# Optimization experiments

Measured on AMD Instinct MI355X. Metric: run time of the kernel, lower is better.

## Reference

```python
import jax, jax.numpy as jnp
import numpy as np

N_HEAD = 16

def rel_shift(x):
    # x: (qlen, klen, B, n). Pad one zero column at front of klen axis,
    # reinterpret as (klen+1, qlen, B, n), drop first row, reshape back.
    qlen, klen, b, n = x.shape
    x_pad = jnp.pad(x, ((0, 0), (1, 0), (0, 0), (0, 0)))
    x_pad = x_pad.reshape(klen + 1, qlen, b, n)
    return x_pad[1:].reshape(qlen, klen, b, n)

def setup_inputs() -> dict:
    key = jax.random.key(0)
    ks = jax.random.split(key, 9)
    qlen = klen = 1024
    B = 4
    d_model = 1024
    d_head = d_model // N_HEAD
    q = jax.random.normal(ks[0], (qlen, B, d_model), jnp.float32)
    K = jax.random.normal(ks[1], (klen, B, d_model), jnp.float32)
    V = jax.random.normal(ks[2], (klen, B, d_model), jnp.float32)
    mask = jax.random.bernoulli(ks[3], 0.1, (1, klen, B, 1))
    r = jax.random.normal(ks[4], (klen, d_model), jnp.float32)
    u = jax.random.normal(ks[5], (N_HEAD, d_head), jnp.float32) * 0.02
    v = jax.random.normal(ks[6], (N_HEAD, d_head), jnp.float32) * 0.02
    Wr = jax.random.normal(ks[7], (d_model, d_model), jnp.float32) / np.sqrt(d_model)
    br = jax.random.normal(ks[8], (d_model,), jnp.float32) * 0.02
    return {"q": q, "K": K, "V": V, "mask": mask, "r": r, "u": u, "v": v, "Wr": Wr, "br": br}

def reference(q, K, V, mask, r, u, v, Wr, br):
    qlen, bsz, d_model = q.shape
    klen = K.shape[0]
    d_head = d_model // N_HEAD
    qh = q.reshape(qlen, bsz, N_HEAD, d_head)
    Kh = K.reshape(klen, bsz, N_HEAD, d_head)
    Vh = V.reshape(klen, bsz, N_HEAD, d_head)
    rh = (r @ Wr.T + br).reshape(klen, N_HEAD, d_head)  # r_net projection
    AC = jnp.einsum('ibnd,jbnd->ijbn', qh + u, Kh)
    BD = rel_shift(jnp.einsum('ibnd,jnd->ijbn', qh + v, rh))
    score = (AC + BD) / jnp.sqrt(jnp.asarray(d_head, q.dtype))
    # mask (1,klen,B,1) broadcasts over qlen and heads (torch repeats over heads)
    score = jnp.where(mask, jnp.asarray(-1e9, score.dtype), score)
    weight = jax.nn.softmax(score, axis=1)
    out = jnp.einsum('ijbn,jbnd->ibnd', weight, Vh).reshape(qlen, bsz, d_model)
    return out, weight.mean(axis=-1)
```

## Files before the change

kernel.cpp:

```cpp
#include <hip/hip_runtime.h>
#include <hip/hip_fp16.h>
#include <stdint.h>


#define L 1024
#define BATCH 4
#define NH 16
#define DH 64
#define DM 1024
#define TI 16
#define NJT 16
#define BDP_ST 1032
#define SCALE 0.125f

typedef __attribute__((ext_vector_type(8))) short short8;
typedef __attribute__((ext_vector_type(4))) float f32x4;

static __device__ __forceinline__ unsigned short f2bf(float f) {
    union { float f; unsigned int u; } x; x.f = f;
    return (unsigned short)((x.u + 0x7fffu + ((x.u >> 16) & 1u)) >> 16);
}
static __device__ __forceinline__ float bf2f(unsigned short h) {
    union { unsigned int u; float f; } x; x.u = ((unsigned int)h) << 16;
    return x.f;
}
static __device__ __forceinline__ unsigned short f2h(float f) {
    __half h = __float2half(f);
    union { __half h; unsigned short s; } x; x.h = h; return x.s;
}
static __device__ __forceinline__ float h2f(unsigned short s) {
    union { __half h; unsigned short s; } x; x.s = s; return __half2float(x.h);
}
static __device__ __forceinline__ unsigned short* usp(void* base, int byteoff) {
    return (unsigned short*)((char*)base + byteoff);
}
static __device__ __forceinline__ short8 ld8(const void* base, int byteoff) {
    return *(const short8*)((const char*)base + byteoff);
}
#define SW128(row, colByte) ((((row) * 128) + (colByte)) ^ (((row) & 7) << 4))

__global__ __launch_bounds__(256) void rh_gemm_kernel(
    const float* __restrict__ r, const float* __restrict__ Wr,
    const float* __restrict__ br, float* __restrict__ rhf,
    unsigned short* __restrict__ rhb, int bfmode)
{
    __shared__ float As[16][65];
    __shared__ float Bs[16][65];
    const int j0 = blockIdx.x * 64;
    const int m0 = blockIdx.y * 64;
    const int tid = threadIdx.x;
    const int ty = tid >> 4, tx = tid & 15;
    float acc[4][4] = {};

    for (int k0 = 0; k0 < DM; k0 += 16) {
        const int row = tid >> 2, c4 = (tid & 3) << 2;
        float4 av = *(const float4*)(r  + (size_t)(j0 + row) * DM + k0 + c4);
        float4 bv = *(const float4*)(Wr + (size_t)(m0 + row) * DM + k0 + c4);
        __syncthreads();
        As[c4 + 0][row] = av.x; As[c4 + 1][row] = av.y;
        As[c4 + 2][row] = av.z; As[c4 + 3][row] = av.w;
        Bs[c4 + 0][row] = bv.x; Bs[c4 + 1][row] = bv.y;
        Bs[c4 + 2][row] = bv.z; Bs[c4 + 3][row] = bv.w;
        __syncthreads();
#pragma unroll
        for (int k = 0; k < 16; ++k) {
            float a[4], bb[4];
#pragma unroll
            for (int t = 0; t < 4; ++t) { a[t] = As[k][ty * 4 + t]; bb[t] = Bs[k][tx * 4 + t]; }
#pragma unroll
            for (int ii = 0; ii < 4; ++ii)
#pragma unroll
                for (int jj = 0; jj < 4; ++jj)
                    acc[ii][jj] = fmaf(a[ii], bb[jj], acc[ii][jj]);
        }
    }
#pragma unroll
    for (int ii = 0; ii < 4; ++ii) {
        const int row = j0 + ty * 4 + ii;
#pragma unroll
        for (int jj = 0; jj < 4; ++jj) {
            const int col = m0 + tx * 4 + jj;
            const float val = acc[ii][jj] + br[col];
            if (bfmode)
                rhb[(((size_t)(col >> 6)) * L + row) * DH + (col & 63)] = f2bf(val);
            else
                rhf[(size_t)row * DM + col] = val;
        }
    }
}

__global__ __launch_bounds__(256) void prepass_kernel(
    const float* __restrict__ Kg, const float* __restrict__ Vg,
    unsigned short* __restrict__ Kbf, unsigned short* __restrict__ Vtb)
{
    __shared__ unsigned short tile[64][80];
    const int j0 = blockIdx.x * 64;
    const int b = blockIdx.y, n = blockIdx.z;
    const int bn = b * NH + n;
    const int tid = threadIdx.x;

    for (int idx = tid; idx < 64 * 16; idx += 256) {
        const int jr = idx >> 4, s4 = (idx & 15) * 4;
        const size_t src = ((size_t)(j0 + jr) * BATCH + b) * DM + n * DH + s4;
        float4 kv = *(const float4*)(Kg + src);
        ushort4 o;
        o.x = f2bf(kv.x); o.y = f2bf(kv.y); o.z = f2bf(kv.z); o.w = f2bf(kv.w);
        *(ushort4*)(Kbf + ((size_t)bn * L + j0 + jr) * DH + s4) = o;
        float4 vv4 = *(const float4*)(Vg + src);
        tile[s4 + 0][jr] = f2bf(vv4.x); tile[s4 + 1][jr] = f2bf(vv4.y);
        tile[s4 + 2][jr] = f2bf(vv4.z); tile[s4 + 3][jr] = f2bf(vv4.w);
    }
    __syncthreads();
    for (int idx = tid; idx < 64 * 8; idx += 256) {
        const int d = idx >> 3, p8 = (idx & 7) * 8;
        short8 o = *(const short8*)&tile[d][p8];
        *(short8*)(Vtb + ((size_t)bn * DH + d) * L + j0 + p8) = o;
    }
}

__global__ __launch_bounds__(256) void wm_reduce_kernel(
    const unsigned short* __restrict__ W_ws, float* __restrict__ wm_out)
{
    const int gi = blockIdx.x;
    const int b  = blockIdx.y;
    const int j0 = threadIdx.x * 4;
    float acc0 = 0.f, acc1 = 0.f, acc2 = 0.f, acc3 = 0.f;
#pragma unroll
    for (int n = 0; n < NH; ++n) {
        ushort4 wv = *(const ushort4*)(W_ws + (((size_t)(b * NH + n) * L + gi) * L) + j0);
        acc0 += bf2f(wv.x); acc1 += bf2f(wv.y);
        acc2 += bf2f(wv.z); acc3 += bf2f(wv.w);
    }
    const size_t o = ((size_t)gi * L + j0) * BATCH + b;
    wm_out[o]             = acc0 * (1.f / 16.f);
    wm_out[o + BATCH]     = acc1 * (1.f / 16.f);
    wm_out[o + 2 * BATCH] = acc2 * (1.f / 16.f);
    wm_out[o + 3 * BATCH] = acc3 * (1.f / 16.f);
}

template<int MODE, int PLAIN>
__global__ __launch_bounds__(256, 2) void attn_kernel(
    const float* __restrict__ q,
    const void* __restrict__ Kp, const void* __restrict__ Vp,
    const unsigned char* __restrict__ maskp,
    const float* __restrict__ uu, const float* __restrict__ vvp,
    const void* __restrict__ rhp,
    float* __restrict__ out, float* __restrict__ wm_out,
    unsigned short* __restrict__ W_ws)
{
    __shared__ unsigned short QU[16 * 64];
    __shared__ unsigned short QV[17 * 64];
    __shared__ unsigned short KR[(MODE == 1) ? 64 * 64 : 8];
    __shared__ unsigned short VT[(MODE == 1) ? 64 * 64 : 8];
    __shared__ unsigned short BDp[17 * BDP_ST];
    __shared__ unsigned short Wt[16 * 64];
    __shared__ unsigned char mblk[L];
    __shared__ float denomP[4][16];
    __shared__ float rdenom[16];
    __shared__ int mflags;

    const int i0 = blockIdx.x * TI;
    const int b  = blockIdx.y;
    const int n  = blockIdx.z;
    const int bn = b * NH + n;
    const int tid = threadIdx.x;
    const int w = tid >> 6, lane = tid & 63, lr = lane & 15, lg = lane >> 4;

    const unsigned short* Kbf = (const unsigned short*)Kp;
    const unsigned short* Vtb = (const unsigned short*)Vp;
    const unsigned short* rhb = (const unsigned short*)rhp;
    const float* Kg  = (const float*)Kp;
    const float* Vg  = (const float*)Vp;
    const float* rhf = (const float*)rhp;

    if (tid == 0) mflags = 0;
    __syncthreads();
    {
        int local = 0;
        for (int ww = tid; ww < 1024; ww += 256) {
            const unsigned int word = ((const unsigned int*)maskp)[ww];
            if (word == 0x3f800000u) local |= 1;
            else if (word & 0xffffff00u) local |= 2;
        }
        if (local) atomicOr(&mflags, local);
    }
    __syncthreads();
    {
        const int mtype = (mflags & 1) ? 2 : ((mflags & 2) ? 1 : 0);
        for (int j = tid; j < L; j += 256) {
            bool mv;
            if (mtype == 2)      mv = ((const float*)maskp)[j * BATCH + b] != 0.f;
            else if (mtype == 1) mv = maskp[j * BATCH + b] != 0;
            else                 mv = ((const int*)maskp)[j * BATCH + b] != 0;
            mblk[j] = mv ? 1 : 0;
        }
    }
    for (int idx = tid; idx < 17 * 64; idx += 256) {
        const int row = idx >> 6, d = idx & 63;
        const int gi = i0 + row;
        const float qval = (gi < L) ? q[((size_t)gi * BATCH + b) * DM + n * DH + d] : 0.f;
        *usp(QV, SW128(row, d * 2)) = f2bf(qval + vvp[n * DH + d]);
        if (row < 16) *usp(QU, SW128(row, d * 2)) = f2bf(qval + uu[n * DH + d]);
    }
    __syncthreads();

    for (int ct = 0; ct < 16; ++ct) {
        const int c0 = ct * 64;
        if constexpr (MODE == 1) {
            __syncthreads();
            for (int idx = tid; idx < 64 * 16; idx += 256) {
                const int cr = idx >> 4, d4 = (idx & 15) * 4;
                float4 rv = *(const float4*)(rhf + (size_t)(c0 + cr) * DM + n * DH + d4);
                unsigned short* p = usp(KR, SW128(cr, d4 * 2));
                p[0] = f2bf(rv.x); p[1] = f2bf(rv.y); p[2] = f2bf(rv.z); p[3] = f2bf(rv.w);
            }
            __syncthreads();
        }
        const int ccol = w * 16 + lr;
        f32x4 acc = {0.f, 0.f, 0.f, 0.f};
#pragma unroll
        for (int kh = 0; kh < 2; ++kh) {
            short8 a = ld8(QV, SW128(lr, (kh * 32 + lg * 8) * 2));
            short8 bb;
            if constexpr (MODE == 0)
                bb = *(const short8*)(rhb + ((size_t)n * L + c0 + ccol) * DH + kh * 32 + lg * 8);
            else
                bb = ld8(KR, SW128(ccol, (kh * 32 + lg * 8) * 2));
            acc = __builtin_amdgcn_mfma_f32_16x16x32_bf16(a, bb, acc, 0, 0, 0);
        }
#pragma unroll
        for (int r2 = 0; r2 < 4; ++r2)
            BDp[(lg * 4 + r2) * BDP_ST + c0 + ccol] = f2h(acc[r2]);
        {
            const int col = tid >> 2, kq = (tid & 3) * 16;
            float s16 = 0.f;
#pragma unroll
            for (int kk = 0; kk < 16; kk += 8) {
                short8 qa = ld8(QV, SW128(16, (kq + kk) * 2));
                short8 ra;
                if constexpr (MODE == 0)
                    ra = *(const short8*)(rhb + ((size_t)n * L + c0 + col) * DH + kq + kk);
                else
                    ra = ld8(KR, SW128(col, (kq + kk) * 2));
#pragma unroll
                for (int e = 0; e < 8; ++e)
                    s16 = fmaf(bf2f((unsigned short)qa[e]), bf2f((unsigned short)ra[e]), s16);
            }
            s16 += __shfl_xor(s16, 1);
            s16 += __shfl_xor(s16, 2);
            if ((tid & 3) == 0) BDp[16 * BDP_ST + c0 + col] = f2h(s16);
        }
    }
    __syncthreads();

    f32x4 pv = {0.f, 0.f, 0.f, 0.f};
    float dl[4] = {0.f, 0.f, 0.f, 0.f};
    float tmp[4][NJT];
    const int jloc = w * 16 + lr;
#pragma unroll
    for (int jt = 0; jt < NJT; ++jt) {
        const int j0 = jt * 64;
        const int gj = j0 + jloc;
        if constexpr (MODE == 1) {
            for (int idx = tid; idx < 64 * 16; idx += 256) {
                const int jr = idx >> 4, d4 = (idx & 15) * 4;
                const size_t src = ((size_t)(j0 + jr) * BATCH + b) * DM + n * DH + d4;
                float4 kv = *(const float4*)(Kg + src);
                unsigned short* p = usp(KR, SW128(jr, d4 * 2));
                p[0] = f2bf(kv.x); p[1] = f2bf(kv.y); p[2] = f2bf(kv.z); p[3] = f2bf(kv.w);
                float4 vv4 = *(const float4*)(Vg + src);
                *usp(VT, SW128(d4 + 0, jr * 2)) = f2bf(vv4.x);
                *usp(VT, SW128(d4 + 1, jr * 2)) = f2bf(vv4.y);
                *usp(VT, SW128(d4 + 2, jr * 2)) = f2bf(vv4.z);
                *usp(VT, SW128(d4 + 3, jr * 2)) = f2bf(vv4.w);
            }
            __syncthreads();
        }
        f32x4 acc = {0.f, 0.f, 0.f, 0.f};
#pragma unroll
        for (int kh = 0; kh < 2; ++kh) {
            short8 a = ld8(QU, SW128(lr, (kh * 32 + lg * 8) * 2));
            short8 bb;
            if constexpr (MODE == 0)
                bb = *(const short8*)(Kbf + ((size_t)bn * L + gj) * DH + kh * 32 + lg * 8);
            else
                bb = ld8(KR, SW128(jloc, (kh * 32 + lg * 8) * 2));
            acc = __builtin_amdgcn_mfma_f32_16x16x32_bf16(a, bb, acc, 0, 0, 0);
        }
        const bool msk = mblk[gj] != 0;
#pragma unroll
        for (int r2 = 0; r2 < 4; ++r2) {
            const int il = lg * 4 + r2;
            const int gi = i0 + il;
            const int t = gj - gi;
            float bd = 0.f;
            if (t != 1) {
                const int c = (t <= 0) ? (L - 1 + t) : (t - 2);
                bd = h2f(BDp[(il + (t >= 1 ? 1 : 0)) * BDP_ST + c]);
            }
            float s = (acc[r2] + bd) * SCALE;
            if (msk) s = -1e9f;
            const float wgt = __expf(fminf(s, 80.f));
            dl[r2] += wgt;
            tmp[r2][jt] = wgt;
            *usp(Wt, SW128(il, jloc * 2)) = f2bf(wgt);
        }
        __syncthreads();
#pragma unroll
        for (int kh = 0; kh < 2; ++kh) {
            short8 a = ld8(Wt, SW128(lr, (kh * 32 + lg * 8) * 2));
            short8 bb;
            if constexpr (MODE == 0)
                bb = *(const short8*)(Vtb + ((size_t)bn * DH + jloc) * L + j0 + kh * 32 + lg * 8);
            else
                bb = ld8(VT, SW128(jloc, (kh * 32 + lg * 8) * 2));
            pv = __builtin_amdgcn_mfma_f32_16x16x32_bf16(a, bb, pv, 0, 0, 0);
        }
        __syncthreads();
    }

#pragma unroll
    for (int r2 = 0; r2 < 4; ++r2) {
        float d = dl[r2];
        d += __shfl_xor(d, 1); d += __shfl_xor(d, 2);
        d += __shfl_xor(d, 4); d += __shfl_xor(d, 8);
        if (lr == 0) denomP[w][lg * 4 + r2] = d;
    }
    __syncthreads();
    if (tid < 16)
        rdenom[tid] = 1.f / (denomP[0][tid] + denomP[1][tid] + denomP[2][tid] + denomP[3][tid]);
    __syncthreads();

#pragma unroll
    for (int r2 = 0; r2 < 4; ++r2) {
        const int il = lg * 4 + r2;
        out[((size_t)(i0 + il) * BATCH + b) * DM + n * DH + w * 16 + lr] = pv[r2] * rdenom[il];
    }

    if constexpr (PLAIN == 1) {
#pragma unroll
        for (int r2 = 0; r2 < 4; ++r2) {
            const int il = lg * 4 + r2;
            const float rs = rdenom[il];
            const size_t rowo = ((size_t)bn * L + i0 + il) * L;
#pragma unroll
            for (int jt = 0; jt < NJT; ++jt)
                W_ws[rowo + jt * 64 + jloc] = f2bf(tmp[r2][jt] * rs);
        }
    } else {
#pragma unroll
        for (int r2 = 0; r2 < 4; ++r2) {
            const int il = lg * 4 + r2;
            const float rs = rdenom[il] * (1.f / 16.f);
#pragma unroll
            for (int jt = 0; jt < NJT; ++jt)
                atomicAdd(wm_out + ((size_t)(i0 + il) * L + jt * 64 + jloc) * BATCH + b,
                          tmp[r2][jt] * rs);
        }
    }
}

extern "C" void kernel_launch(void* const* d_in, const int* in_sizes, int n_in,
                              void* d_out, int out_size, void* d_ws, size_t ws_size,
                              hipStream_t stream)
{
    (void)in_sizes; (void)n_in; (void)out_size;
    const float* q   = (const float*)d_in[0];
    const float* K   = (const float*)d_in[1];
    const float* V   = (const float*)d_in[2];
    const unsigned char* mask = (const unsigned char*)d_in[3];
    const float* r   = (const float*)d_in[4];
    const float* u   = (const float*)d_in[5];
    const float* v   = (const float*)d_in[6];
    const float* Wr  = (const float*)d_in[7];
    const float* br  = (const float*)d_in[8];

    float* out = (float*)d_out;
    float* wm  = out + (size_t)L * BATCH * DM;

    const size_t kvbytes = (size_t)BATCH * NH * L * DH * 2;
    const size_t rhbytes = (size_t)NH * L * DH * 2;
    const size_t wmbytes = (size_t)BATCH * NH * L * L * 2;

    if (ws_size >= 2 * kvbytes + rhbytes + wmbytes) {
        unsigned short* Kbf = (unsigned short*)d_ws;
        unsigned short* Vtb = Kbf + kvbytes / 2;
        unsigned short* rhb = Vtb + kvbytes / 2;
        unsigned short* Wws = rhb + rhbytes / 2;
        rh_gemm_kernel<<<dim3(16, 16), 256, 0, stream>>>(r, Wr, br, nullptr, rhb, 1);
        prepass_kernel<<<dim3(16, 4, 16), 256, 0, stream>>>(K, V, Kbf, Vtb);
        attn_kernel<0, 1><<<dim3(64, 4, 16), 256, 0, stream>>>(
            q, Kbf, Vtb, mask, u, v, rhb, out, wm, Wws);
        wm_reduce_kernel<<<dim3(L, BATCH), 256, 0, stream>>>(Wws, wm);
    } else if (ws_size >= 2 * kvbytes + rhbytes) {
        hipMemsetAsync(wm, 0, (size_t)L * L * BATCH * sizeof(float), stream);
        unsigned short* Kbf = (unsigned short*)d_ws;
        unsigned short* Vtb = Kbf + kvbytes / 2;
        unsigned short* rhb = Vtb + kvbytes / 2;
        rh_gemm_kernel<<<dim3(16, 16), 256, 0, stream>>>(r, Wr, br, nullptr, rhb, 1);
        prepass_kernel<<<dim3(16, 4, 16), 256, 0, stream>>>(K, V, Kbf, Vtb);
        attn_kernel<0, 0><<<dim3(64, 4, 16), 256, 0, stream>>>(
            q, Kbf, Vtb, mask, u, v, rhb, out, wm, nullptr);
    } else {
        hipMemsetAsync(wm, 0, (size_t)L * L * BATCH * sizeof(float), stream);
        float* rhf = (float*)d_ws;
        rh_gemm_kernel<<<dim3(16, 16), 256, 0, stream>>>(r, Wr, br, rhf, nullptr, 0);
        attn_kernel<1, 0><<<dim3(64, 4, 16), 256, 0, stream>>>(
            q, K, V, mask, u, v, rhf, out, wm, nullptr);
    }
}
```

Baseline: 356.6 us.

## Register double-buffer K/V/rh fragments and double-buffer Wt to drop a barrier

Prefetches the next tile's K, V and rh MFMA fragments into registers (ping-pong buffers) in the default mode, so global loads overlap the current tile's compute. Wt shared tile is double-buffered, which removes the trailing __syncthreads per j-tile. The 1/sqrt(d) scale is folded into QU/QV at load time instead of multiplying each score. Launch bounds raised to 3 blocks per CU, which constrains registers and may cause spills given the extra prefetch registers and the tmp array.

```diff
diff --git a/kernel.cpp b/kernel.cpp
--- a/kernel.cpp
+++ b/kernel.cpp
@@ -139,7 +139,7 @@
 }
 
 template<int MODE, int PLAIN>
-__global__ __launch_bounds__(256, 2) void attn_kernel(
+__global__ __launch_bounds__(256, 3) void attn_kernel(
     const float* __restrict__ q,
     const void* __restrict__ Kp, const void* __restrict__ Vp,
     const unsigned char* __restrict__ maskp,
@@ -153,7 +153,7 @@
     __shared__ unsigned short KR[(MODE == 1) ? 64 * 64 : 8];
     __shared__ unsigned short VT[(MODE == 1) ? 64 * 64 : 8];
     __shared__ unsigned short BDp[17 * BDP_ST];
-    __shared__ unsigned short Wt[16 * 64];
+    __shared__ unsigned short Wt[2][16 * 64];
     __shared__ unsigned char mblk[L];
     __shared__ float denomP[4][16];
     __shared__ float rdenom[16];
@@ -199,56 +199,79 @@
         const int row = idx >> 6, d = idx & 63;
         const int gi = i0 + row;
         const float qval = (gi < L) ? q[((size_t)gi * BATCH + b) * DM + n * DH + d] : 0.f;
-        *usp(QV, SW128(row, d * 2)) = f2bf(qval + vvp[n * DH + d]);
-        if (row < 16) *usp(QU, SW128(row, d * 2)) = f2bf(qval + uu[n * DH + d]);
-    }
-    __syncthreads();
-
-    for (int ct = 0; ct < 16; ++ct) {
-        const int c0 = ct * 64;
-        if constexpr (MODE == 1) {
-            __syncthreads();
-            for (int idx = tid; idx < 64 * 16; idx += 256) {
-                const int cr = idx >> 4, d4 = (idx & 15) * 4;
-                float4 rv = *(const float4*)(rhf + (size_t)(c0 + cr) * DM + n * DH + d4);
-                unsigned short* p = usp(KR, SW128(cr, d4 * 2));
-                p[0] = f2bf(rv.x); p[1] = f2bf(rv.y); p[2] = f2bf(rv.z); p[3] = f2bf(rv.w);
-            }
-            __syncthreads();
-        }
-        const int ccol = w * 16 + lr;
-        f32x4 acc = {0.f, 0.f, 0.f, 0.f};
+        *usp(QV, SW128(row, d * 2)) = f2bf((qval + vvp[n * DH + d]) * SCALE);
+        if (row < 16) *usp(QU, SW128(row, d * 2)) = f2bf((qval + uu[n * DH + d]) * SCALE);
+    }
+    __syncthreads();
+
+    {
+        short8 rb[2][2];
+        if constexpr (MODE == 0) {
+#pragma unroll
+            for (int kh = 0; kh < 2; ++kh)
+                rb[0][kh] = *(const short8*)(rhb + ((size_t)n * L + w * 16 + lr) * DH + kh * 32 + lg * 8);
+        }
+#pragma unroll
+        for (int ct = 0; ct < 16; ++ct) {
+            const int c0 = ct * 64;
+            const int ccol = w * 16 + lr;
+            if constexpr (MODE == 0) {
+                if (ct + 1 < 16) {
+#pragma unroll
+                    for (int kh = 0; kh < 2; ++kh)
+                        rb[(ct + 1) & 1][kh] = *(const short8*)(rhb + ((size_t)n * L + (ct + 1) * 64 + ccol) * DH + kh * 32 + lg * 8);
+                }
+            } else {
+                __syncthreads();
+                for (int idx = tid; idx < 64 * 16; idx += 256) {
+                    const int cr = idx >> 4, d4 = (idx & 15) * 4;
+                    float4 rv = *(const float4*)(rhf + (size_t)(c0 + cr) * DM + n * DH + d4);
+                    unsigned short* p = usp(KR, SW128(cr, d4 * 2));
+                    p[0] = f2bf(rv.x); p[1] = f2bf(rv.y); p[2] = f2bf(rv.z); p[3] = f2bf(rv.w);
+                }
+                __syncthreads();
+            }
+            f32x4 acc = {0.f, 0.f, 0.f, 0.f};
+#pragma unroll
+            for (int kh = 0; kh < 2; ++kh) {
+                short8 a = ld8(QV, SW128(lr, (kh * 32 + lg * 8) * 2));
+                short8 bb;
+                if constexpr (MODE == 0) bb = rb[ct & 1][kh];
+                else                     bb = ld8(KR, SW128(ccol, (kh * 32 + lg * 8) * 2));
+                acc = __builtin_amdgcn_mfma_f32_16x16x32_bf16(a, bb, acc, 0, 0, 0);
+            }
+#pragma unroll
+            for (int r2 = 0; r2 < 4; ++r2)
+                BDp[(lg * 4 + r2) * BDP_ST + c0 + ccol] = f2h(acc[r2]);
+            {
+                const int col = tid >> 2, kq = (tid & 3) * 16;
+                float s16 = 0.f;
+#pragma unroll
+                for (int kk = 0; kk < 16; kk += 8) {
+                    short8 qa = ld8(QV, SW128(16, (kq + kk) * 2));
+                    short8 ra;
+                    if constexpr (MODE == 0)
+                        ra = *(const short8*)(rhb + ((size_t)n * L + c0 + col) * DH + kq + kk);
+                    else
+                        ra = ld8(KR, SW128(col, (kq + kk) * 2));
+#pragma unroll
+                    for (int e = 0; e < 8; ++e)
+                        s16 = fmaf(bf2f((unsigned short)qa[e]), bf2f((unsigned short)ra[e]), s16);
+                }
+                s16 += __shfl_xor(s16, 1);
+                s16 += __shfl_xor(s16, 2);
+                if ((tid & 3) == 0) BDp[16 * BDP_ST + c0 + col] = f2h(s16);
+            }
+        }
+    }
+
+    const int jloc = w * 16 + lr;
+    short8 kf[2][2], vf[2][2];
+    if constexpr (MODE == 0) {
 #pragma unroll
         for (int kh = 0; kh < 2; ++kh) {
-            short8 a = ld8(QV, SW128(lr, (kh * 32 + lg * 8) * 2));
-            short8 bb;
-            if constexpr (MODE == 0)
-                bb = *(const short8*)(rhb + ((size_t)n * L + c0 + ccol) * DH + kh * 32 + lg * 8);
-            else
-                bb = ld8(KR, SW128(ccol, (kh * 32 + lg * 8) * 2));
-            acc = __builtin_amdgcn_mfma_f32_16x16x32_bf16(a, bb, acc, 0, 0, 0);
-        }
-#pragma unroll
-        for (int r2 = 0; r2 < 4; ++r2)
-            BDp[(lg * 4 + r2) * BDP_ST + c0 + ccol] = f2h(acc[r2]);
-        {
-            const int col = tid >> 2, kq = (tid & 3) * 16;
-            float s16 = 0.f;
-#pragma unroll
-            for (int kk = 0; kk < 16; kk += 8) {
-                short8 qa = ld8(QV, SW128(16, (kq + kk) * 2));
-                short8 ra;
-                if constexpr (MODE == 0)
-                    ra = *(const short8*)(rhb + ((size_t)n * L + c0 + col) * DH + kq + kk);
-                else
-                    ra = ld8(KR, SW128(col, (kq + kk) * 2));
-#pragma unroll
-                for (int e = 0; e < 8; ++e)
-                    s16 = fmaf(bf2f((unsigned short)qa[e]), bf2f((unsigned short)ra[e]), s16);
-            }
-            s16 += __shfl_xor(s16, 1);
-            s16 += __shfl_xor(s16, 2);
-            if ((tid & 3) == 0) BDp[16 * BDP_ST + c0 + col] = f2h(s16);
+            kf[0][kh] = *(const short8*)(Kbf + ((size_t)bn * L + jloc) * DH + kh * 32 + lg * 8);
+            vf[0][kh] = *(const short8*)(Vtb + ((size_t)bn * DH + jloc) * L + kh * 32 + lg * 8);
         }
     }
     __syncthreads();
@@ -256,12 +279,22 @@
     f32x4 pv = {0.f, 0.f, 0.f, 0.f};
     float dl[4] = {0.f, 0.f, 0.f, 0.f};
     float tmp[4][NJT];
-    const int jloc = w * 16 + lr;
 #pragma unroll
     for (int jt = 0; jt < NJT; ++jt) {
         const int j0 = jt * 64;
         const int gj = j0 + jloc;
-        if constexpr (MODE == 1) {
+        const int cur = jt & 1;
+        if constexpr (MODE == 0) {
+            if (jt + 1 < NJT) {
+                const int j0n = (jt + 1) * 64;
+#pragma unroll
+                for (int kh = 0; kh < 2; ++kh) {
+                    kf[cur ^ 1][kh] = *(const short8*)(Kbf + ((size_t)bn * L + j0n + jloc) * DH + kh * 32 + lg * 8);
+                    vf[cur ^ 1][kh] = *(const short8*)(Vtb + ((size_t)bn * DH + jloc) * L + j0n + kh * 32 + lg * 8);
+                }
+            }
+        } else {
+            __syncthreads();
             for (int idx = tid; idx < 64 * 16; idx += 256) {
                 const int jr = idx >> 4, d4 = (idx & 15) * 4;
                 const size_t src = ((size_t)(j0 + jr) * BATCH + b) * DM + n * DH + d4;
@@ -281,10 +314,8 @@
         for (int kh = 0; kh < 2; ++kh) {
             short8 a = ld8(QU, SW128(lr, (kh * 32 + lg * 8) * 2));
             short8 bb;
-            if constexpr (MODE == 0)
-                bb = *(const short8*)(Kbf + ((size_t)bn * L + gj) * DH + kh * 32 + lg * 8);
-            else
-                bb = ld8(KR, SW128(jloc, (kh * 32 + lg * 8) * 2));
+            if constexpr (MODE == 0) bb = kf[cur][kh];
+            else                     bb = ld8(KR, SW128(jloc, (kh * 32 + lg * 8) * 2));
             acc = __builtin_amdgcn_mfma_f32_16x16x32_bf16(a, bb, acc, 0, 0, 0);
         }
         const bool msk = mblk[gj] != 0;
@@ -298,25 +329,22 @@
                 const int c = (t <= 0) ? (L - 1 + t) : (t - 2);
                 bd = h2f(BDp[(il + (t >= 1 ? 1 : 0)) * BDP_ST + c]);
             }
-            float s = (acc[r2] + bd) * SCALE;
+            float s = acc[r2] + bd;
             if (msk) s = -1e9f;
             const float wgt = __expf(fminf(s, 80.f));
             dl[r2] += wgt;
             tmp[r2][jt] = wgt;
-            *usp(Wt, SW128(il, jloc * 2)) = f2bf(wgt);
+            *usp(Wt[cur], SW128(il, jloc * 2)) = f2bf(wgt);
         }
         __syncthreads();
 #pragma unroll
         for (int kh = 0; kh < 2; ++kh) {
-            short8 a = ld8(Wt, SW128(lr, (kh * 32 + lg * 8) * 2));
+            short8 a = ld8(Wt[cur], SW128(lr, (kh * 32 + lg * 8) * 2));
             short8 bb;
-            if constexpr (MODE == 0)
-                bb = *(const short8*)(Vtb + ((size_t)bn * DH + jloc) * L + j0 + kh * 32 + lg * 8);
-            else
-                bb = ld8(VT, SW128(jloc, (kh * 32 + lg * 8) * 2));
+            if constexpr (MODE == 0) bb = vf[cur][kh];
+            else                     bb = ld8(VT, SW128(jloc, (kh * 32 + lg * 8) * 2));
             pv = __builtin_amdgcn_mfma_f32_16x16x32_bf16(a, bb, pv, 0, 0, 0);
         }
-        __syncthreads();
     }
 
 #pragma unroll
```

New measurement: 342.1 us. 4.1% less time.
